# Optimization experiments

Measured on AMD Instinct MI355X. Metric: run time of the kernel, lower is better.

The kernel has to match this reference:

```python
import jax, jax.numpy as jnp
import numpy as np

TEMPERATURE = 8.0  # sqrt(head_dim=64)

def setup_inputs() -> dict:
    key = jax.random.key(0)
    kq, kk, kv, km = jax.random.split(key, 4)
    B, H, S, D = 2, 16, 2048, 64
    return {
        "query": jax.random.normal(kq, (B, H, S, D), dtype=jnp.float32),
        "key": jax.random.normal(kk, (B, H, S, D), dtype=jnp.float32),
        "value": jax.random.normal(kv, (B, H, S, D), dtype=jnp.float32),
        "mask": jax.random.randint(km, (B, S, S), 0, 2, dtype=jnp.int32),
    }

def reference(query, key, value, mask):
    # energy: [B, H, Sq, Skv]
    energy = jnp.einsum("bhqd,bhkd->bhqk", query, key) / TEMPERATURE
    # mask broadcast over heads; positions where mask == 0 get -10000
    energy = jnp.where(mask[:, None, :, :] == 0, jnp.float32(-10000.0), energy)
    attention = jax.nn.softmax(energy, axis=-1)
    # replicate the module's NaN cleanup (softmax over all -inf rows)
    attention = jnp.where(jnp.isnan(attention), jnp.float32(0.0), attention)
    # dropout is identity in eval/deterministic mode
    out = jnp.einsum("bhqk,bhkd->bhqd", attention, value)
    return out, attention
```

## Files before the change

kernel.cpp:

```cpp
#include <hip/hip_runtime.h>

typedef __attribute__((ext_vector_type(8))) short short8;
typedef __attribute__((ext_vector_type(4))) float floatx4;

#define MFMA16(a, b, c) __builtin_amdgcn_mfma_f32_16x16x32_bf16((a), (b), (c), 0, 0, 0)

static constexpr int Bn = 2, Hn = 16, Sn = 2048, Dn = 64;
static constexpr int QT = 64;
static constexpr int KT = 32;
static constexpr int NIT = Sn / KT;
static constexpr int KS_LD = 72;
static constexpr int VT_LD = 40;
static constexpr int PS_LD = 40;

__device__ __forceinline__ ushort f2bf(float f) {
    union { float f; unsigned int u; } c; c.f = f;
    unsigned int u = c.u;
    u += 0x7FFFu + ((u >> 16) & 1u);
    return (ushort)(u >> 16);
}

__device__ __forceinline__ short8 pack8(float4 a, float4 b) {
    short8 r;
    r[0] = (short)f2bf(a.x); r[1] = (short)f2bf(a.y);
    r[2] = (short)f2bf(a.z); r[3] = (short)f2bf(a.w);
    r[4] = (short)f2bf(b.x); r[5] = (short)f2bf(b.y);
    r[6] = (short)f2bf(b.z); r[7] = (short)f2bf(b.w);
    return r;
}

__device__ __forceinline__ void wg_barrier() {
    asm volatile("s_waitcnt lgkmcnt(0)" ::: "memory");
    __builtin_amdgcn_s_barrier();
    asm volatile("" ::: "memory");
}

__global__ __launch_bounds__(256, 4) void sdpa_kernel(
    const float* __restrict__ Q,
    const float* __restrict__ K,
    const float* __restrict__ V,
    const int*   __restrict__ M,
    float* __restrict__ O,
    float* __restrict__ A)
{
    const int qt = blockIdx.x, h = blockIdx.y, b = blockIdx.z;
    const int tid  = threadIdx.x;
    const int wave = tid >> 6;
    const int lane = tid & 63;
    const int l16  = lane & 15;
    const int quad = lane >> 4;
    const int l16h = l16 >> 3;
    const int l7   = l16 & 7;

    const size_t head = (size_t)(b * Hn + h) * Sn * Dn;
    const float* Qh = Q + head;
    const float* Kh = K + head;
    const float* Vh = V + head;
    const int qg0 = qt * QT + wave * 16;
    const int* Mb = M + (size_t)b * Sn * Sn;
    float* Ahead = A + (size_t)(b * Hn + h) * Sn * Sn;
    float* Ohead = O + head;

    __shared__ short KsA[2][KT * KS_LD];
    __shared__ short VTb[2][Dn * VT_LD];
    __shared__ short Ps[4][16 * PS_LD];

    short8 qf[2];
    {
        const float* qp = Qh + (size_t)(qg0 + l16) * Dn;
        qf[0] = pack8(*(const float4*)(qp + quad * 8), *(const float4*)(qp + quad * 8 + 4));
        qf[1] = pack8(*(const float4*)(qp + 32 + quad * 8), *(const float4*)(qp + 36 + quad * 8));
    }

    const int srow = tid >> 3;
    const int scol = (tid & 7) * 8;
    const int vidx = (((tid >> 6) ^ (tid & 3)) << 3) + (srow & 7);

    const int* Mrow[4];
    float* Arow[4];
    #pragma unroll
    for (int r = 0; r < 4; ++r) {
        const int row = qg0 + quad * 4 + r;
        Mrow[r] = Mb + (size_t)row * Sn;
        Arow[r] = Ahead + (size_t)row * Sn;
    }

    unsigned long long mA[4]    = {0ull, 0ull, 0ull, 0ull};
    unsigned long long mroll[4] = {0ull, 0ull, 0ull, 0ull};

    float psum[4] = {0.f, 0.f, 0.f, 0.f};
    {
        const float* kst = Kh + (size_t)srow * Dn + scol;
        {
            float4 a = *(const float4*)kst;
            float4 c = *(const float4*)(kst + 4);
            *(short8*)&KsA[0][srow * KS_LD + scol] = pack8(a, c);
        }
        kst += KT * Dn;
        float4 ka = *(const float4*)kst;
        float4 kb = *(const float4*)(kst + 4);
        kst += KT * Dn;
        __syncthreads();

        short* kc = KsA[0];
        short* kn = KsA[1];
        for (int it = 0; it < NIT; ++it) {
            if (it + 1 < NIT)
                *(short8*)&kn[srow * KS_LD + scol] = pack8(ka, kb);
            if (it + 2 < NIT) {
                ka = *(const float4*)kst;
                kb = *(const float4*)(kst + 4);
                kst += KT * Dn;
            }

            floatx4 z = {0.f, 0.f, 0.f, 0.f};
            floatx4 sc[2] = {z, z};
            #pragma unroll
            for (int t = 0; t < 2; ++t)
                #pragma unroll
                for (int c = 0; c < 2; ++c) {
                    short8 kf = *(const short8*)&kc[(t * 16 + l16) * KS_LD + c * 32 + quad * 8];
                    sc[t] = MFMA16(qf[c], kf, sc[t]);
                }

            const int col0 = it * KT + l16;
            int mv0[4], mv1[4];
            #pragma unroll
            for (int r = 0; r < 4; ++r) {
                mv0[r] = Mrow[r][col0];
                mv1[r] = Mrow[r][col0 + 16];
            }

            wg_barrier();

            #pragma unroll
            for (int r = 0; r < 4; ++r) {
                const float e0 = mv0[r] ? sc[0][r] * 0.125f : -10000.0f;
                const float e1 = mv1[r] ? sc[1][r] * 0.125f : -10000.0f;
                psum[r] += __expf(e0) + __expf(e1);
                const unsigned long long bits =
                    (unsigned long long)((mv0[r] ? 1u : 0u) | (mv1[r] ? 2u : 0u));
                mroll[r] = (mroll[r] >> 2) | (bits << 62);
            }
            if (it == 31) {
                mA[0] = mroll[0]; mA[1] = mroll[1]; mA[2] = mroll[2]; mA[3] = mroll[3];
            }
            short* tmp = kc; kc = kn; kn = tmp;
        }
    }

    float invl[4];
    #pragma unroll
    for (int r = 0; r < 4; ++r) {
        float s = psum[r];
        #pragma unroll
        for (int off = 1; off < 16; off <<= 1)
            s += __shfl_xor(s, off);
        invl[r] = s > 0.f ? 1.0f / s : 0.f;
    }

    floatx4 z0 = {0.f, 0.f, 0.f, 0.f};
    floatx4 oacc[4] = {z0, z0, z0, z0};
    {
        const float* kst = Kh + (size_t)srow * Dn + scol;
        const float* vst = Vh + (size_t)srow * Dn + scol;
        {
            float4 a = *(const float4*)kst;  float4 c = *(const float4*)(kst + 4);
            *(short8*)&KsA[0][srow * KS_LD + scol] = pack8(a, c);
            float4 d = *(const float4*)vst;  float4 e = *(const float4*)(vst + 4);
            short* vp = &VTb[0][scol * VT_LD + vidx];
            vp[0 * VT_LD] = (short)f2bf(d.x); vp[1 * VT_LD] = (short)f2bf(d.y);
            vp[2 * VT_LD] = (short)f2bf(d.z); vp[3 * VT_LD] = (short)f2bf(d.w);
            vp[4 * VT_LD] = (short)f2bf(e.x); vp[5 * VT_LD] = (short)f2bf(e.y);
            vp[6 * VT_LD] = (short)f2bf(e.z); vp[7 * VT_LD] = (short)f2bf(e.w);
        }
        kst += KT * Dn; vst += KT * Dn;
        float4 ka = *(const float4*)kst, kb = *(const float4*)(kst + 4);
        float4 va = *(const float4*)vst, vb = *(const float4*)(vst + 4);
        kst += KT * Dn; vst += KT * Dn;
        __syncthreads();

        short* kc = KsA[0]; short* kn = KsA[1];
        short* vc = VTb[0]; short* vn = VTb[1];
        short* psw = Ps[wave];
        const int psr = l16 * PS_LD + ((quad ^ ((l16 >> 2) & 3)) << 3);

        for (int it = 0; it < NIT; ++it) {
            if (it + 1 < NIT) {
                *(short8*)&kn[srow * KS_LD + scol] = pack8(ka, kb);
                short* vp = &vn[scol * VT_LD + vidx];
                vp[0 * VT_LD] = (short)f2bf(va.x); vp[1 * VT_LD] = (short)f2bf(va.y);
                vp[2 * VT_LD] = (short)f2bf(va.z); vp[3 * VT_LD] = (short)f2bf(va.w);
                vp[4 * VT_LD] = (short)f2bf(vb.x); vp[5 * VT_LD] = (short)f2bf(vb.y);
                vp[6 * VT_LD] = (short)f2bf(vb.z); vp[7 * VT_LD] = (short)f2bf(vb.w);
            }
            if (it + 2 < NIT) {
                ka = *(const float4*)kst; kb = *(const float4*)(kst + 4);
                va = *(const float4*)vst; vb = *(const float4*)(vst + 4);
                kst += KT * Dn; vst += KT * Dn;
            }
            if (it == 32) {
                mA[0] = mroll[0]; mA[1] = mroll[1]; mA[2] = mroll[2]; mA[3] = mroll[3];
            }

            floatx4 z = {0.f, 0.f, 0.f, 0.f};
            floatx4 sc[2] = {z, z};
            #pragma unroll
            for (int t = 0; t < 2; ++t)
                #pragma unroll
                for (int c = 0; c < 2; ++c) {
                    short8 kf = *(const short8*)&kc[(t * 16 + l16) * KS_LD + c * 32 + quad * 8];
                    sc[t] = MFMA16(qf[c], kf, sc[t]);
                }

            const int col0 = it * KT + l16;
            #pragma unroll
            for (int r = 0; r < 4; ++r) {
                const int m0 = (int)mA[r] & 1;
                const int m1 = (int)mA[r] & 2;
                mA[r] >>= 2;
                const float e0 = m0 ? sc[0][r] * 0.125f : -10000.0f;
                const float e1 = m1 ? sc[1][r] * 0.125f : -10000.0f;
                const float p0 = __expf(e0) * invl[r];
                const float p1 = __expf(e1) * invl[r];
                Arow[r][col0]      = p0;
                Arow[r][col0 + 16] = p1;
                const int prow = (quad * 4 + r) * PS_LD;
                psw[prow + (((0 + l16h) ^ quad) << 3) + l7] = (short)f2bf(p0);
                psw[prow + (((2 + l16h) ^ quad) << 3) + l7] = (short)f2bf(p1);
            }
            asm volatile("s_waitcnt lgkmcnt(0)" ::: "memory");

            short8 pf = *(const short8*)&psw[psr];
            #pragma unroll
            for (int tn = 0; tn < 4; ++tn) {
                const int pbv = (quad ^ ((2 * tn + l16h) & 3)) << 3;
                short8 vf = *(const short8*)&vc[(tn * 16 + l16) * VT_LD + pbv];
                oacc[tn] = MFMA16(pf, vf, oacc[tn]);
            }

            wg_barrier();
            short* t1 = kc; kc = kn; kn = t1;
            short* t2 = vc; vc = vn; vn = t2;
        }
    }

    #pragma unroll
    for (int tn = 0; tn < 4; ++tn)
        #pragma unroll
        for (int r = 0; r < 4; ++r)
            Ohead[(size_t)(qg0 + quad * 4 + r) * Dn + tn * 16 + l16] = oacc[tn][r];
}

extern "C" void kernel_launch(void* const* d_in, const int* in_sizes, int n_in,
                              void* d_out, int out_size, void* d_ws, size_t ws_size,
                              hipStream_t stream) {
    const float* Q = (const float*)d_in[0];
    const float* K = (const float*)d_in[1];
    const float* V = (const float*)d_in[2];
    const int*   M = (const int*)d_in[3];
    float* O = (float*)d_out;
    float* A = O + (size_t)Bn * Hn * Sn * Dn;
    dim3 grid(Sn / QT, Hn, Bn);
    sdpa_kernel<<<grid, 256, 0, stream>>>(Q, K, V, M, O, A);
}
```

Baseline: 794.9 us.

## Fuse row-sum pass into PV pass and normalize output at the end

Merges the separate softmax-denominator pass into the P·V pass, accumulating unnormalized probabilities into the output and dividing by the row sum only at the end. No max is subtracted, so this relies on the exp values staying in range, just as the old two-pass code did. A third pass recomputes QK^T using K loaded straight from global memory into registers, with no LDS and no barriers, and writes the normalized attention matrix with nontemporal stores. This saves one full shared-memory K pipeline and its barriers, but P is rounded to bf16 before normalization rather than after.

```diff
diff --git a/kernel.cpp b/kernel.cpp
--- a/kernel.cpp
+++ b/kernel.cpp
@@ -89,76 +89,6 @@
     unsigned long long mroll[4] = {0ull, 0ull, 0ull, 0ull};
 
     float psum[4] = {0.f, 0.f, 0.f, 0.f};
-    {
-        const float* kst = Kh + (size_t)srow * Dn + scol;
-        {
-            float4 a = *(const float4*)kst;
-            float4 c = *(const float4*)(kst + 4);
-            *(short8*)&KsA[0][srow * KS_LD + scol] = pack8(a, c);
-        }
-        kst += KT * Dn;
-        float4 ka = *(const float4*)kst;
-        float4 kb = *(const float4*)(kst + 4);
-        kst += KT * Dn;
-        __syncthreads();
-
-        short* kc = KsA[0];
-        short* kn = KsA[1];
-        for (int it = 0; it < NIT; ++it) {
-            if (it + 1 < NIT)
-                *(short8*)&kn[srow * KS_LD + scol] = pack8(ka, kb);
-            if (it + 2 < NIT) {
-                ka = *(const float4*)kst;
-                kb = *(const float4*)(kst + 4);
-                kst += KT * Dn;
-            }
-
-            floatx4 z = {0.f, 0.f, 0.f, 0.f};
-            floatx4 sc[2] = {z, z};
-            #pragma unroll
-            for (int t = 0; t < 2; ++t)
-                #pragma unroll
-                for (int c = 0; c < 2; ++c) {
-                    short8 kf = *(const short8*)&kc[(t * 16 + l16) * KS_LD + c * 32 + quad * 8];
-                    sc[t] = MFMA16(qf[c], kf, sc[t]);
-                }
-
-            const int col0 = it * KT + l16;
-            int mv0[4], mv1[4];
-            #pragma unroll
-            for (int r = 0; r < 4; ++r) {
-                mv0[r] = Mrow[r][col0];
-                mv1[r] = Mrow[r][col0 + 16];
-            }
-
-            wg_barrier();
-
-            #pragma unroll
-            for (int r = 0; r < 4; ++r) {
-                const float e0 = mv0[r] ? sc[0][r] * 0.125f : -10000.0f;
-                const float e1 = mv1[r] ? sc[1][r] * 0.125f : -10000.0f;
-                psum[r] += __expf(e0) + __expf(e1);
-                const unsigned long long bits =
-                    (unsigned long long)((mv0[r] ? 1u : 0u) | (mv1[r] ? 2u : 0u));
-                mroll[r] = (mroll[r] >> 2) | (bits << 62);
-            }
-            if (it == 31) {
-                mA[0] = mroll[0]; mA[1] = mroll[1]; mA[2] = mroll[2]; mA[3] = mroll[3];
-            }
-            short* tmp = kc; kc = kn; kn = tmp;
-        }
-    }
-
-    float invl[4];
-    #pragma unroll
-    for (int r = 0; r < 4; ++r) {
-        float s = psum[r];
-        #pragma unroll
-        for (int off = 1; off < 16; off <<= 1)
-            s += __shfl_xor(s, off);
-        invl[r] = s > 0.f ? 1.0f / s : 0.f;
-    }
-
     floatx4 z0 = {0.f, 0.f, 0.f, 0.f};
     floatx4 oacc[4] = {z0, z0, z0, z0};
     {
@@ -199,9 +129,6 @@
                 va = *(const float4*)vst; vb = *(const float4*)(vst + 4);
                 kst += KT * Dn; vst += KT * Dn;
             }
-            if (it == 32) {
-                mA[0] = mroll[0]; mA[1] = mroll[1]; mA[2] = mroll[2]; mA[3] = mroll[3];
-            }
 
             floatx4 z = {0.f, 0.f, 0.f, 0.f};
             floatx4 sc[2] = {z, z};
@@ -212,6 +139,107 @@
                     short8 kf = *(const short8*)&kc[(t * 16 + l16) * KS_LD + c * 32 + quad * 8];
                     sc[t] = MFMA16(qf[c], kf, sc[t]);
                 }
+
+            const int col0 = it * KT + l16;
+            int mv0[4], mv1[4];
+            #pragma unroll
+            for (int r = 0; r < 4; ++r) {
+                mv0[r] = Mrow[r][col0];
+                mv1[r] = Mrow[r][col0 + 16];
+            }
+
+            #pragma unroll
+            for (int r = 0; r < 4; ++r) {
+                const float e0 = mv0[r] ? sc[0][r] * 0.125f : -10000.0f;
+                const float e1 = mv1[r] ? sc[1][r] * 0.125f : -10000.0f;
+                const float pt0 = __expf(e0);
+                const float pt1 = __expf(e1);
+                psum[r] += pt0 + pt1;
+                const unsigned long long bits =
+                    (unsigned long long)((mv0[r] ? 1u : 0u) | (mv1[r] ? 2u : 0u));
+                mroll[r] = (mroll[r] >> 2) | (bits << 62);
+                const int prow = (quad * 4 + r) * PS_LD;
+                psw[prow + (((0 + l16h) ^ quad) << 3) + l7] = (short)f2bf(pt0);
+                psw[prow + (((2 + l16h) ^ quad) << 3) + l7] = (short)f2bf(pt1);
+            }
+            if (it == 31) {
+                mA[0] = mroll[0]; mA[1] = mroll[1]; mA[2] = mroll[2]; mA[3] = mroll[3];
+            }
+
+            asm volatile("s_waitcnt lgkmcnt(0)" ::: "memory");
+
+            short8 pf = *(const short8*)&psw[psr];
+            #pragma unroll
+            for (int tn = 0; tn < 4; ++tn) {
+                const int pbv = (quad ^ ((2 * tn + l16h) & 3)) << 3;
+                short8 vf = *(const short8*)&vc[(tn * 16 + l16) * VT_LD + pbv];
+                oacc[tn] = MFMA16(pf, vf, oacc[tn]);
+            }
+
+            wg_barrier();
+            short* t1 = kc; kc = kn; kn = t1;
+            short* t2 = vc; vc = vn; vn = t2;
+        }
+    }
+
+    float invl[4];
+    #pragma unroll
+    for (int r = 0; r < 4; ++r) {
+        float s = psum[r];
+        #pragma unroll
+        for (int off = 1; off < 16; off <<= 1)
+            s += __shfl_xor(s, off);
+        invl[r] = s > 0.f ? 1.0f / s : 0.f;
+    }
+
+    #pragma unroll
+    for (int tn = 0; tn < 4; ++tn)
+        #pragma unroll
+        for (int r = 0; r < 4; ++r)
+            Ohead[(size_t)(qg0 + quad * 4 + r) * Dn + tn * 16 + l16] = oacc[tn][r] * invl[r];
+
+    {
+        float4 f[2][2][2];
+        #pragma unroll
+        for (int t = 0; t < 2; ++t)
+            #pragma unroll
+            for (int c = 0; c < 2; ++c) {
+                const float* p = Kh + (size_t)(t * 16 + l16) * Dn + c * 32 + quad * 8;
+                f[t][c][0] = *(const float4*)p;
+                f[t][c][1] = *(const float4*)(p + 4);
+            }
+
+        for (int it = 0; it < NIT; ++it) {
+            short8 kf[2][2];
+            #pragma unroll
+            for (int t = 0; t < 2; ++t)
+                #pragma unroll
+                for (int c = 0; c < 2; ++c)
+                    kf[t][c] = pack8(f[t][c][0], f[t][c][1]);
+
+            if (it + 1 < NIT) {
+                #pragma unroll
+                for (int t = 0; t < 2; ++t)
+                    #pragma unroll
+                    for (int c = 0; c < 2; ++c) {
+                        const float* p = Kh + (size_t)((it + 1) * KT + t * 16 + l16) * Dn
+                                            + c * 32 + quad * 8;
+                        f[t][c][0] = *(const float4*)p;
+                        f[t][c][1] = *(const float4*)(p + 4);
+                    }
+            }
+
+            floatx4 z = {0.f, 0.f, 0.f, 0.f};
+            floatx4 sc[2] = {z, z};
+            #pragma unroll
+            for (int t = 0; t < 2; ++t)
+                #pragma unroll
+                for (int c = 0; c < 2; ++c)
+                    sc[t] = MFMA16(qf[c], kf[t][c], sc[t]);
+
+            if (it == 32) {
+                mA[0] = mroll[0]; mA[1] = mroll[1]; mA[2] = mroll[2]; mA[3] = mroll[3];
+            }
 
             const int col0 = it * KT + l16;
             #pragma unroll
@@ -223,33 +251,11 @@
                 const float e1 = m1 ? sc[1][r] * 0.125f : -10000.0f;
                 const float p0 = __expf(e0) * invl[r];
                 const float p1 = __expf(e1) * invl[r];
-                Arow[r][col0]      = p0;
-                Arow[r][col0 + 16] = p1;
-                const int prow = (quad * 4 + r) * PS_LD;
-                psw[prow + (((0 + l16h) ^ quad) << 3) + l7] = (short)f2bf(p0);
-                psw[prow + (((2 + l16h) ^ quad) << 3) + l7] = (short)f2bf(p1);
-            }
-            asm volatile("s_waitcnt lgkmcnt(0)" ::: "memory");
-
-            short8 pf = *(const short8*)&psw[psr];
-            #pragma unroll
-            for (int tn = 0; tn < 4; ++tn) {
-                const int pbv = (quad ^ ((2 * tn + l16h) & 3)) << 3;
-                short8 vf = *(const short8*)&vc[(tn * 16 + l16) * VT_LD + pbv];
-                oacc[tn] = MFMA16(pf, vf, oacc[tn]);
-            }
-
-            wg_barrier();
-            short* t1 = kc; kc = kn; kn = t1;
-            short* t2 = vc; vc = vn; vn = t2;
+                __builtin_nontemporal_store(p0, &Arow[r][col0]);
+                __builtin_nontemporal_store(p1, &Arow[r][col0 + 16]);
+            }
         }
     }
-
-    #pragma unroll
-    for (int tn = 0; tn < 4; ++tn)
-        #pragma unroll
-        for (int r = 0; r < 4; ++r)
-            Ohead[(size_t)(qg0 + quad * 4 + r) * Dn + tn * 16 + l16] = oacc[tn][r];
 }
 
 extern "C" void kernel_launch(void* const* d_in, const int* in_sizes, int n_in,
```

Result: slower. 853.2 us (+7.3%).

## Transpose QK MFMA so P stays in registers, defer normalization, vectorize mask/attention I/O

Applied to the files above, without the earlier changes.

Swaps MFMA operand order so each lane holds four consecutive key columns of one query row. Unnormalized exp values then feed the PV MFMA directly as 16x16x16 bf16 operands, with no LDS round trip for P. The first pass now does QK^T, exp and PV together, and the output is scaled by the row sum afterwards. A second QK pass writes normalized attention with float4 stores and int4 mask loads. The point is to remove the P staging through LDS and to replace scalar mask reads and attention writes with vector ones. The cost is more PV MFMA instructions and unchanged total QK recompute.

```diff
diff --git a/kernel.cpp b/kernel.cpp
--- a/kernel.cpp
+++ b/kernel.cpp
@@ -1,9 +1,11 @@
 #include <hip/hip_runtime.h>
 
 typedef __attribute__((ext_vector_type(8))) short short8;
+typedef __attribute__((ext_vector_type(4))) short bf16x4;
 typedef __attribute__((ext_vector_type(4))) float floatx4;
 
-#define MFMA16(a, b, c) __builtin_amdgcn_mfma_f32_16x16x32_bf16((a), (b), (c), 0, 0, 0)
+#define MFMA_QK(a, b, c) __builtin_amdgcn_mfma_f32_16x16x32_bf16((a), (b), (c), 0, 0, 0)
+#define MFMA_PV(a, b, c) __builtin_amdgcn_mfma_f32_16x16x16bf16_1k((a), (b), (c), 0, 0, 0)
 
 static constexpr int Bn = 2, Hn = 16, Sn = 2048, Dn = 64;
 static constexpr int QT = 64;
@@ -11,7 +13,6 @@
 static constexpr int NIT = Sn / KT;
 static constexpr int KS_LD = 72;
 static constexpr int VT_LD = 40;
-static constexpr int PS_LD = 40;
 
 __device__ __forceinline__ ushort f2bf(float f) {
     union { float f; unsigned int u; } c; c.f = f;
@@ -50,7 +51,6 @@
     const int l16  = lane & 15;
     const int quad = lane >> 4;
     const int l16h = l16 >> 3;
-    const int l7   = l16 & 7;
 
     const size_t head = (size_t)(b * Hn + h) * Sn * Dn;
     const float* Qh = Q + head;
@@ -63,7 +63,6 @@
 
     __shared__ short KsA[2][KT * KS_LD];
     __shared__ short VTb[2][Dn * VT_LD];
-    __shared__ short Ps[4][16 * PS_LD];
 
     short8 qf[2];
     {
@@ -76,89 +75,10 @@
     const int scol = (tid & 7) * 8;
     const int vidx = (((tid >> 6) ^ (tid & 3)) << 3) + (srow & 7);
 
-    const int* Mrow[4];
-    float* Arow[4];
-    #pragma unroll
-    for (int r = 0; r < 4; ++r) {
-        const int row = qg0 + quad * 4 + r;
-        Mrow[r] = Mb + (size_t)row * Sn;
-        Arow[r] = Ahead + (size_t)row * Sn;
-    }
-
-    unsigned long long mA[4]    = {0ull, 0ull, 0ull, 0ull};
-    unsigned long long mroll[4] = {0ull, 0ull, 0ull, 0ull};
-
-    float psum[4] = {0.f, 0.f, 0.f, 0.f};
-    {
-        const float* kst = Kh + (size_t)srow * Dn + scol;
-        {
-            float4 a = *(const float4*)kst;
-            float4 c = *(const float4*)(kst + 4);
-            *(short8*)&KsA[0][srow * KS_LD + scol] = pack8(a, c);
-        }
-        kst += KT * Dn;
-        float4 ka = *(const float4*)kst;
-        float4 kb = *(const float4*)(kst + 4);
-        kst += KT * Dn;
-        __syncthreads();
-
-        short* kc = KsA[0];
-        short* kn = KsA[1];
-        for (int it = 0; it < NIT; ++it) {
-            if (it + 1 < NIT)
-                *(short8*)&kn[srow * KS_LD + scol] = pack8(ka, kb);
-            if (it + 2 < NIT) {
-                ka = *(const float4*)kst;
-                kb = *(const float4*)(kst + 4);
-                kst += KT * Dn;
-            }
-
-            floatx4 z = {0.f, 0.f, 0.f, 0.f};
-            floatx4 sc[2] = {z, z};
-            #pragma unroll
-            for (int t = 0; t < 2; ++t)
-                #pragma unroll
-                for (int c = 0; c < 2; ++c) {
-                    short8 kf = *(const short8*)&kc[(t * 16 + l16) * KS_LD + c * 32 + quad * 8];
-                    sc[t] = MFMA16(qf[c], kf, sc[t]);
-                }
-
-            const int col0 = it * KT + l16;
-            int mv0[4], mv1[4];
-            #pragma unroll
-            for (int r = 0; r < 4; ++r) {
-                mv0[r] = Mrow[r][col0];
-                mv1[r] = Mrow[r][col0 + 16];
-            }
-
-            wg_barrier();
-
-            #pragma unroll
-            for (int r = 0; r < 4; ++r) {
-                const float e0 = mv0[r] ? sc[0][r] * 0.125f : -10000.0f;
-                const float e1 = mv1[r] ? sc[1][r] * 0.125f : -10000.0f;
-                psum[r] += __expf(e0) + __expf(e1);
-                const unsigned long long bits =
-                    (unsigned long long)((mv0[r] ? 1u : 0u) | (mv1[r] ? 2u : 0u));
-                mroll[r] = (mroll[r] >> 2) | (bits << 62);
-            }
-            if (it == 31) {
-                mA[0] = mroll[0]; mA[1] = mroll[1]; mA[2] = mroll[2]; mA[3] = mroll[3];
-            }
-            short* tmp = kc; kc = kn; kn = tmp;
-        }
-    }
-
-    float invl[4];
-    #pragma unroll
-    for (int r = 0; r < 4; ++r) {
-        float s = psum[r];
-        #pragma unroll
-        for (int off = 1; off < 16; off <<= 1)
-            s += __shfl_xor(s, off);
-        invl[r] = s > 0.f ? 1.0f / s : 0.f;
-    }
-
+    const int* Mrow0 = Mb + (size_t)(qg0 + l16) * Sn;
+    float* Arow0 = Ahead + (size_t)(qg0 + l16) * Sn;
+
+    float psum = 0.f;
     floatx4 z0 = {0.f, 0.f, 0.f, 0.f};
     floatx4 oacc[4] = {z0, z0, z0, z0};
     {
@@ -182,8 +102,6 @@
 
         short* kc = KsA[0]; short* kn = KsA[1];
         short* vc = VTb[0]; short* vn = VTb[1];
-        short* psw = Ps[wave];
-        const int psr = l16 * PS_LD + ((quad ^ ((l16 >> 2) & 3)) << 3);
 
         for (int it = 0; it < NIT; ++it) {
             if (it + 1 < NIT) {
@@ -199,9 +117,6 @@
                 va = *(const float4*)vst; vb = *(const float4*)(vst + 4);
                 kst += KT * Dn; vst += KT * Dn;
             }
-            if (it == 32) {
-                mA[0] = mroll[0]; mA[1] = mroll[1]; mA[2] = mroll[2]; mA[3] = mroll[3];
-            }
 
             floatx4 z = {0.f, 0.f, 0.f, 0.f};
             floatx4 sc[2] = {z, z};
@@ -210,33 +125,39 @@
                 #pragma unroll
                 for (int c = 0; c < 2; ++c) {
                     short8 kf = *(const short8*)&kc[(t * 16 + l16) * KS_LD + c * 32 + quad * 8];
-                    sc[t] = MFMA16(qf[c], kf, sc[t]);
+                    sc[t] = MFMA_QK(kf, qf[c], sc[t]);
                 }
 
-            const int col0 = it * KT + l16;
-            #pragma unroll
-            for (int r = 0; r < 4; ++r) {
-                const int m0 = (int)mA[r] & 1;
-                const int m1 = (int)mA[r] & 2;
-                mA[r] >>= 2;
-                const float e0 = m0 ? sc[0][r] * 0.125f : -10000.0f;
-                const float e1 = m1 ? sc[1][r] * 0.125f : -10000.0f;
-                const float p0 = __expf(e0) * invl[r];
-                const float p1 = __expf(e1) * invl[r];
-                Arow[r][col0]      = p0;
-                Arow[r][col0 + 16] = p1;
-                const int prow = (quad * 4 + r) * PS_LD;
-                psw[prow + (((0 + l16h) ^ quad) << 3) + l7] = (short)f2bf(p0);
-                psw[prow + (((2 + l16h) ^ quad) << 3) + l7] = (short)f2bf(p1);
-            }
-            asm volatile("s_waitcnt lgkmcnt(0)" ::: "memory");
-
-            short8 pf = *(const short8*)&psw[psr];
+            const int* mrp = Mrow0 + it * KT + (quad << 2);
+            const int4 m0 = *(const int4*)mrp;
+            const int4 m1 = *(const int4*)(mrp + 16);
+
+            float pt0[4], pt1[4];
+            pt0[0] = __expf(m0.x ? sc[0][0] * 0.125f : -10000.0f);
+            pt0[1] = __expf(m0.y ? sc[0][1] * 0.125f : -10000.0f);
+            pt0[2] = __expf(m0.z ? sc[0][2] * 0.125f : -10000.0f);
+            pt0[3] = __expf(m0.w ? sc[0][3] * 0.125f : -10000.0f);
+            pt1[0] = __expf(m1.x ? sc[1][0] * 0.125f : -10000.0f);
+            pt1[1] = __expf(m1.y ? sc[1][1] * 0.125f : -10000.0f);
+            pt1[2] = __expf(m1.z ? sc[1][2] * 0.125f : -10000.0f);
+            pt1[3] = __expf(m1.w ? sc[1][3] * 0.125f : -10000.0f);
+            psum += (pt0[0] + pt0[1]) + (pt0[2] + pt0[3])
+                  + (pt1[0] + pt1[1]) + (pt1[2] + pt1[3]);
+
+            bf16x4 af0 = { (short)f2bf(pt0[0]), (short)f2bf(pt0[1]),
+                           (short)f2bf(pt0[2]), (short)f2bf(pt0[3]) };
+            bf16x4 af1 = { (short)f2bf(pt1[0]), (short)f2bf(pt1[1]),
+                           (short)f2bf(pt1[2]), (short)f2bf(pt1[3]) };
+
             #pragma unroll
             for (int tn = 0; tn < 4; ++tn) {
-                const int pbv = (quad ^ ((2 * tn + l16h) & 3)) << 3;
-                short8 vf = *(const short8*)&vc[(tn * 16 + l16) * VT_LD + pbv];
-                oacc[tn] = MFMA16(pf, vf, oacc[tn]);
+                const int row = tn * 16 + l16;
+                const int dg  = (2 * tn + l16h) & 3;
+                const int base = row * VT_LD + ((quad & 1) << 2);
+                bf16x4 vf0 = *(const bf16x4*)&vc[base + ((((quad >> 1)) ^ dg) << 3)];
+                oacc[tn] = MFMA_PV(af0, vf0, oacc[tn]);
+                bf16x4 vf1 = *(const bf16x4*)&vc[base + (((2 + (quad >> 1)) ^ dg) << 3)];
+                oacc[tn] = MFMA_PV(af1, vf1, oacc[tn]);
             }
 
             wg_barrier();
@@ -245,11 +166,73 @@
         }
     }
 
+    float s = psum;
+    s += __shfl_xor(s, 16);
+    s += __shfl_xor(s, 32);
+    const float invl = s > 0.f ? 1.0f / s : 0.f;
+
+    float invo[4];
+    #pragma unroll
+    for (int r = 0; r < 4; ++r) invo[r] = __shfl(invl, (quad << 2) + r);
     #pragma unroll
     for (int tn = 0; tn < 4; ++tn)
         #pragma unroll
         for (int r = 0; r < 4; ++r)
-            Ohead[(size_t)(qg0 + quad * 4 + r) * Dn + tn * 16 + l16] = oacc[tn][r];
+            Ohead[(size_t)(qg0 + (quad << 2) + r) * Dn + tn * 16 + l16] =
+                oacc[tn][r] * invo[r];
+
+    {
+        const float* kst = Kh + (size_t)srow * Dn + scol;
+        {
+            float4 a = *(const float4*)kst;  float4 c = *(const float4*)(kst + 4);
+            *(short8*)&KsA[0][srow * KS_LD + scol] = pack8(a, c);
+        }
+        kst += KT * Dn;
+        float4 ka = *(const float4*)kst, kb = *(const float4*)(kst + 4);
+        kst += KT * Dn;
+        __syncthreads();
+
+        short* kc = KsA[0]; short* kn = KsA[1];
+
+        for (int it = 0; it < NIT; ++it) {
+            if (it + 1 < NIT)
+                *(short8*)&kn[srow * KS_LD + scol] = pack8(ka, kb);
+            if (it + 2 < NIT) {
+                ka = *(const float4*)kst; kb = *(const float4*)(kst + 4);
+                kst += KT * Dn;
+            }
+
+            floatx4 z = {0.f, 0.f, 0.f, 0.f};
+            floatx4 sc[2] = {z, z};
+            #pragma unroll
+            for (int t = 0; t < 2; ++t)
+                #pragma unroll
+                for (int c = 0; c < 2; ++c) {
+                    short8 kf = *(const short8*)&kc[(t * 16 + l16) * KS_LD + c * 32 + quad * 8];
+                    sc[t] = MFMA_QK(kf, qf[c], sc[t]);
+                }
+
+            const int* mrp = Mrow0 + it * KT + (quad << 2);
+            const int4 m0 = *(const int4*)mrp;
+            const int4 m1 = *(const int4*)(mrp + 16);
+
+            float4 p0, p1;
+            p0.x = __expf(m0.x ? sc[0][0] * 0.125f : -10000.0f) * invl;
+            p0.y = __expf(m0.y ? sc[0][1] * 0.125f : -10000.0f) * invl;
+            p0.z = __expf(m0.z ? sc[0][2] * 0.125f : -10000.0f) * invl;
+            p0.w = __expf(m0.w ? sc[0][3] * 0.125f : -10000.0f) * invl;
+            p1.x = __expf(m1.x ? sc[1][0] * 0.125f : -10000.0f) * invl;
+            p1.y = __expf(m1.y ? sc[1][1] * 0.125f : -10000.0f) * invl;
+            p1.z = __expf(m1.z ? sc[1][2] * 0.125f : -10000.0f) * invl;
+            p1.w = __expf(m1.w ? sc[1][3] * 0.125f : -10000.0f) * invl;
+
+            *(float4*)&Arow0[it * KT + (quad << 2)]      = p0;
+            *(float4*)&Arow0[it * KT + 16 + (quad << 2)] = p1;
+
+            wg_barrier();
+            short* t1 = kc; kc = kn; kn = t1;
+        }
+    }
 }
 
 extern "C" void kernel_launch(void* const* d_in, const int* in_sizes, int n_in,
```

Result: no change. 802.3 us (+0.9%).
